# Performance work log

Measured on AMD Instinct MI355X. Metric: run time of the kernel, lower is better.

The kernel has to match this reference:

```python
import jax, jax.numpy as jnp
import numpy as np

DIM = 768
HEADS = 12
HEAD_DIM = DIM // HEADS
SCALE = HEAD_DIM ** (-0.5)


def setup_inputs() -> dict:
    key = jax.random.key(0)
    k1, k2, k3 = jax.random.split(key, 3)
    x = jax.random.normal(k1, (4, 2048, DIM), dtype=jnp.float32)
    # nn.Linear(dim, 3*dim, bias=False): weight [3*dim, dim]
    w_qkv = jax.random.normal(k2, (3 * DIM, DIM), dtype=jnp.float32) * (DIM ** -0.5)
    # nn.Linear(dim, dim) with bias
    w_proj = jax.random.normal(k3, (DIM, DIM), dtype=jnp.float32) * (DIM ** -0.5)
    b_proj = jnp.zeros((DIM,), dtype=jnp.float32)
    return {"x": x, "w_qkv": w_qkv, "w_proj": w_proj, "b_proj": b_proj}


def reference(x, w_qkv, w_proj, b_proj):
    B, N, C = x.shape
    H, D = HEADS, HEAD_DIM
    qkv = jnp.einsum('bnc,oc->bno', x, w_qkv)  # [B,N,3C]
    qkv = qkv.reshape(B, N, 3, H, D).transpose(2, 0, 3, 1, 4)  # [3,B,H,N,D]
    q, k, v = qkv[0], qkv[1], qkv[2]
    attn = jnp.einsum('bhnd,bhmd->bhnm', q, k) * SCALE  # [B,H,N,N]
    attn = jax.nn.softmax(attn, axis=-1)
    attn = jax.nn.softmax(attn, axis=-1)  # double softmax, as in original
    out = jnp.einsum('bhnm,bhmd->bhnd', attn, v)  # [B,H,N,D]
    out = out.transpose(0, 2, 1, 3).reshape(B, N, C)
    return jnp.einsum('bnc,oc->bno', out, w_proj) + b_proj
```

## Files before the change

kernel.cpp:

```cpp
#include <hip/hip_runtime.h>
#include <hip/hip_bf16.h>

#define DIM 768
#define HEADS 12
#define HD 64
#define SEQ 2048
#define BATCH 4
#define BHN 48
#define TOK 8192

#if __has_builtin(__builtin_amdgcn_exp2f)
#define EXP2F __builtin_amdgcn_exp2f
#else
#define EXP2F exp2f
#endif
#define EXP_C 0.1803368801111244f

using short8  = __attribute__((ext_vector_type(8))) short;
using short4v = __attribute__((ext_vector_type(4))) short;
using float4v = __attribute__((ext_vector_type(4))) float;

__device__ __forceinline__ short f2b(float f) {
    union { float f; unsigned u; } v; v.f = f;
    unsigned r = v.u + 0x7FFF + ((v.u >> 16) & 1);
    return (short)(r >> 16);
}
__device__ __forceinline__ float b2f(short s) {
    union { unsigned u; float f; } v;
    v.u = ((unsigned)(unsigned short)s) << 16;
    return v.f;
}
__device__ __forceinline__ unsigned pk2(float a, float b) {
    unsigned r;
    asm("v_cvt_pk_bf16_f32 %0, %1, %2" : "=v"(r) : "v"(a), "v"(b));
    return r;
}

typedef const __attribute__((address_space(1))) unsigned GU;
typedef __attribute__((address_space(3))) unsigned LU;
__device__ __forceinline__ void gload_lds16(const short* g, short* l) {
    __builtin_amdgcn_global_load_lds((GU*)g, (LU*)l, 16, 0, 0);
}

__global__ void cast_all(const float* __restrict__ x, const float* __restrict__ wq,
                         const float* __restrict__ wp,
                         short* __restrict__ xb, short* __restrict__ wqb,
                         short* __restrict__ wpb, float* __restrict__ Vsum,
                         int nx4, int nq4) {
    int i = blockIdx.x * 256 + threadIdx.x;
    if (i < BHN * 64) Vsum[i] = 0.f;
    const float* in; short* out; int j = i;
    if (i < nx4)            { in = x;  out = xb;  }
    else if (i < nx4 + nq4) { in = wq; out = wqb; j = i - nx4; }
    else                    { in = wp; out = wpb; j = i - nx4 - nq4; }
    float4 f = ((const float4*)in)[j];
    short4 o;
    o.x = f2b(f.x); o.y = f2b(f.y); o.z = f2b(f.z); o.w = f2b(f.w);
    ((short4*)out)[j] = o;
}

__global__ __launch_bounds__(256, 3)
void gemm_qkv(const short* __restrict__ A, const short* __restrict__ Bw,
              short* __restrict__ Qw, short* __restrict__ Kw, short* __restrict__ Vw,
              float* __restrict__ Vsum)
{
    __shared__ __align__(16) short As[3][128 * 32];
    __shared__ __align__(16) short Bs[3][128 * 32];

    const int tid  = threadIdx.x;
    const int lane = tid & 63;
    const int wave = tid >> 6;
    const int wm = (wave >> 1) * 64, wn = (wave & 1) * 64;
    const int l15 = lane & 15, quad = lane >> 4;

    const int gid = blockIdx.x;
    const int w   = gid >> 3;
    const int ybl = (gid & 7) * 8 + (w & 7);
    const int xbl = w >> 3;

    const bool vpart = (xbl >= 12);
    const short* rowsP = vpart ? (Bw + 1536 * 768) : A;
    const short* colsP = vpart ? A : Bw;
    const int m0 = vpart ? (xbl - 12) * 128 : ybl * 128;
    const int n0 = vpart ? ybl * 128 : xbl * 128;
    const int K = DIM;

    float4v acc[4][4];
    #pragma unroll
    for (int i = 0; i < 4; i++)
        #pragma unroll
        for (int j = 0; j < 4; j++)
            acc[i][j] = (float4v){0.f, 0.f, 0.f, 0.f};

    const int G0 = wave * 128 + lane;
    const int G1 = G0 + 64;
    const int rA0 = G0 >> 2, cA0 = (G0 & 3) * 8;
    const int rA1 = G1 >> 2, cA1 = (G1 & 3) * 8;
    const int ldsoff = wave * 1024;

    auto STAGE = [&](int t, int buf) {
        const int kc = t * 32;
        gload_lds16(&rowsP[(size_t)(m0 + rA0) * K + kc + cA0], &As[buf][ldsoff]);
        gload_lds16(&rowsP[(size_t)(m0 + rA1) * K + kc + cA1], &As[buf][ldsoff + 512]);
        gload_lds16(&colsP[(size_t)(n0 + rA0) * K + kc + cA0], &Bs[buf][ldsoff]);
        gload_lds16(&colsP[(size_t)(n0 + rA1) * K + kc + cA1], &Bs[buf][ldsoff + 512]);
    };

    STAGE(0, 0);
    STAGE(1, 1);

    int cur = 0, nx2 = 2;
    for (int t = 0; t < 24; t++) {
        if (t < 23) { asm volatile("s_waitcnt vmcnt(4)" ::: "memory"); }
        else        { asm volatile("s_waitcnt vmcnt(0)" ::: "memory"); }
        __builtin_amdgcn_sched_barrier(0);
        __builtin_amdgcn_s_barrier();
        __builtin_amdgcn_sched_barrier(0);

        short8 af[4], bfr[4];
        #pragma unroll
        for (int tt = 0; tt < 4; tt++) {
            af[tt]  = *(const short8*)&As[cur][(wm + tt * 16 + l15) * 32 + quad * 8];
            bfr[tt] = *(const short8*)&Bs[cur][(wn + tt * 16 + l15) * 32 + quad * 8];
        }
        #pragma unroll
        for (int tm = 0; tm < 4; tm++)
            #pragma unroll
            for (int tn = 0; tn < 4; tn++)
                acc[tm][tn] = __builtin_amdgcn_mfma_f32_16x16x32_bf16(af[tm], bfr[tn], acc[tm][tn], 0, 0, 0);

        if (t < 22) STAGE(t + 2, nx2);
        cur = (cur == 2) ? 0 : cur + 1;
        nx2 = (nx2 == 2) ? 0 : nx2 + 1;
    }

    #pragma unroll
    for (int tm = 0; tm < 4; tm++)
        #pragma unroll
        for (int tn = 0; tn < 4; tn++)
            #pragma unroll
            for (int r = 0; r < 4; r++) {
                int row = m0 + wm + tm * 16 + quad * 4 + r;
                int col = n0 + wn + tn * 16 + l15;
                float v = acc[tm][tn][r];
                if (vpart) {
                    int hh = row >> 6, d = row & 63;
                    int b = col >> 11, n = col & 2047;
                    int bh = b * HEADS + hh;
                    int t2 = n >> 6, c2h = (n >> 5) & 1, wk = n & 31;
                    int slot = ((wk & 15) >> 2) * 8 + ((wk & 16) >> 2) + (wk & 3);
                    int g2 = c2h * 4 + (slot >> 3);
                    int gp2 = g2 ^ (d & 7);
                    Vw[(size_t)bh * (SEQ * 64) + t2 * 4096 + d * 64 + gp2 * 8 + (slot & 7)] = f2b(v);
                } else {
                    int hh = (col & 767) >> 6, d = col & 63;
                    int b = row >> 11, n = row & 2047;
                    int bh = b * HEADS + hh;
                    size_t idx = (size_t)bh * (SEQ * 64) + (size_t)n * 64
                               + (((d >> 3) ^ (n & 7)) << 3) + (d & 7);
                    if (col < 768) Qw[idx] = f2b(v * EXP_C);
                    else           Kw[idx] = f2b(v);
                }
            }

    if (vpart) {
        const int bb = n0 >> 11;
        #pragma unroll
        for (int tm = 0; tm < 4; tm++)
            #pragma unroll
            for (int r = 0; r < 4; r++) {
                float s4 = (acc[tm][0][r] + acc[tm][1][r]) + (acc[tm][2][r] + acc[tm][3][r]);
                #pragma unroll
                for (int m = 1; m < 16; m <<= 1) s4 += __shfl_xor(s4, m, 64);
                if (l15 == 0) {
                    int row = m0 + wm + tm * 16 + quad * 4 + r;
                    int hh = row >> 6, d = row & 63;
                    atomicAdd(&Vsum[(bb * HEADS + hh) * 64 + d], s4);
                }
            }
    }
}

__global__ __launch_bounds__(256, 4)
void gemm_proj(const short* __restrict__ A, const short* __restrict__ Bw,
               const float* __restrict__ bias, float* __restrict__ Out)
{
    __shared__ __align__(16) short As[3][128 * 32];
    __shared__ __align__(16) short Bs[3][64 * 32];

    const int tid  = threadIdx.x;
    const int lane = tid & 63;
    const int wave = tid >> 6;
    const int wm = (wave >> 1) * 64, wn = (wave & 1) * 32;
    const int l15 = lane & 15, quad = lane >> 4;

    const int gid = blockIdx.x;
    const int w   = gid >> 3;
    const int ybl = (gid & 7) * 8 + (w & 7);
    const int xbl = w >> 3;
    const int m0 = ybl * 128, n0 = xbl * 64;
    const int K = DIM;

    float4v acc[4][2];
    #pragma unroll
    for (int i = 0; i < 4; i++)
        #pragma unroll
        for (int j = 0; j < 2; j++)
            acc[i][j] = (float4v){0.f, 0.f, 0.f, 0.f};

    const int GA0 = wave * 128 + lane, GA1 = GA0 + 64;
    const int rA0 = GA0 >> 2, cA0 = (GA0 & 3) * 8;
    const int rA1 = GA1 >> 2, cA1 = (GA1 & 3) * 8;
    const int GB0 = wave * 64 + lane;
    const int rB0 = GB0 >> 2, cB0 = (GB0 & 3) * 8;
    const int ldsoffA = wave * 1024, ldsoffB = wave * 512;

    auto STAGE = [&](int t, int buf) {
        const int kc = t * 32;
        gload_lds16(&A [(size_t)(m0 + rA0) * K + kc + cA0], &As[buf][ldsoffA]);
        gload_lds16(&A [(size_t)(m0 + rA1) * K + kc + cA1], &As[buf][ldsoffA + 512]);
        gload_lds16(&Bw[(size_t)(n0 + rB0) * K + kc + cB0], &Bs[buf][ldsoffB]);
    };

    STAGE(0, 0);
    STAGE(1, 1);

    int cur = 0, nx2 = 2;
    for (int t = 0; t < 24; t++) {
        if (t < 23) { asm volatile("s_waitcnt vmcnt(3)" ::: "memory"); }
        else        { asm volatile("s_waitcnt vmcnt(0)" ::: "memory"); }
        __builtin_amdgcn_sched_barrier(0);
        __builtin_amdgcn_s_barrier();
        __builtin_amdgcn_sched_barrier(0);

        short8 af[4], bfr[2];
        #pragma unroll
        for (int tt = 0; tt < 4; tt++)
            af[tt] = *(const short8*)&As[cur][(wm + tt * 16 + l15) * 32 + quad * 8];
        #pragma unroll
        for (int tt = 0; tt < 2; tt++)
            bfr[tt] = *(const short8*)&Bs[cur][(wn + tt * 16 + l15) * 32 + quad * 8];
        #pragma unroll
        for (int tm = 0; tm < 4; tm++)
            #pragma unroll
            for (int tn = 0; tn < 2; tn++)
                acc[tm][tn] = __builtin_amdgcn_mfma_f32_16x16x32_bf16(af[tm], bfr[tn], acc[tm][tn], 0, 0, 0);

        if (t < 22) STAGE(t + 2, nx2);
        cur = (cur == 2) ? 0 : cur + 1;
        nx2 = (nx2 == 2) ? 0 : nx2 + 1;
    }

    #pragma unroll
    for (int tm = 0; tm < 4; tm++)
        #pragma unroll
        for (int tn = 0; tn < 2; tn++)
            #pragma unroll
            for (int r = 0; r < 4; r++) {
                int row = m0 + wm + tm * 16 + quad * 4 + r;
                int col = n0 + wn + tn * 16 + l15;
                Out[(size_t)row * 768 + col] = acc[tm][tn][r] + bias[col];
            }
}

__global__ __launch_bounds__(256, 3)
void attn_kernel(const short* __restrict__ Qw, const short* __restrict__ Kw,
                 const short* __restrict__ Vw, const float* __restrict__ Vsum,
                 short* __restrict__ Ow)
{
    __shared__ __align__(16) short LDS[24576];

    const int tid  = threadIdx.x;
    const int lane = tid & 63, wave = tid >> 6;
    const int l15 = lane & 15, quad = lane >> 4;
    const int r7  = l15 & 7;
    const int bid = blockIdx.x;
    const int ii  = bid >> 3;
    const int bh  = (bid & 7) * 6 + (ii >> 4);
    const int qt  = ii & 15;
    const int wq  = wave * 32;

    const short* Qp = Qw + (size_t)bh * (SEQ * 64) + qt * 8192;
    const short* Kp = Kw + (size_t)bh * (SEQ * 64);
    const short* Vp = Vw + (size_t)bh * (SEQ * 64);

    short8 onesf;
    #pragma unroll
    for (int j = 0; j < 8; j++) onesf[j] = (l15 == 0) ? (short)0x3F80 : (short)0;

    #pragma unroll
    for (int h = 0; h < 4; h++) {
        const int g = wave * 4 + h;
        gload_lds16(&Qp[g * 512 + lane * 8], &LDS[g * 512]);
    }
    __syncthreads();
    short8 aq[2][2];
    #pragma unroll
    for (int nb = 0; nb < 2; nb++)
        #pragma unroll
        for (int kk = 0; kk < 2; kk++) {
            int r = wq + nb * 16 + l15;
            aq[nb][kk] = *(const short8*)&LDS[r * 64 + (((kk * 4 + quad) ^ r7) << 3)];
        }
    __syncthreads();

    float4v Aacc[2][4], Lacc[2];
    #pragma unroll
    for (int mb = 0; mb < 2; mb++) {
        Lacc[mb] = (float4v){0.f, 0.f, 0.f, 0.f};
        #pragma unroll
        for (int t = 0; t < 4; t++) Aacc[mb][t] = (float4v){0.f, 0.f, 0.f, 0.f};
    }

    auto STAGE = [&](int t2, int kbuf) {
        const int kb = kbuf * 4096;
        #pragma unroll
        for (int h = 0; h < 2; h++) {
            const int g = wave * 2 + h;
            gload_lds16(&Kp[(size_t)t2 * 4096 + g * 512 + lane * 8], &LDS[kb + g * 512]);
            gload_lds16(&Vp[(size_t)t2 * 4096 + g * 512 + lane * 8], &LDS[12288 + kb + g * 512]);
        }
    };

    STAGE(0, 0);
    STAGE(1, 1);

    int cur = 0, nx2 = 2;
    for (int kt = 0; kt < 32; kt++) {
        if (kt < 31) { asm volatile("s_waitcnt vmcnt(4)" ::: "memory"); }
        else         { asm volatile("s_waitcnt vmcnt(0)" ::: "memory"); }
        __builtin_amdgcn_sched_barrier(0);
        __builtin_amdgcn_s_barrier();
        __builtin_amdgcn_sched_barrier(0);

        const short* KB = &LDS[cur * 4096];
        const short* VB = &LDS[12288 + cur * 4096];

        #pragma unroll
        for (int c2 = 0; c2 < 2; c2++) {
            union AE { unsigned u[4]; short8 s; };
            AE ae[2];
            #pragma unroll
            for (int tn2 = 0; tn2 < 2; tn2++) {
                const int row = (c2 * 2 + tn2) * 16 + l15;
                const short* rp = &KB[row * 64];
                short8 b0 = *(const short8*)&rp[(quad ^ r7) << 3];
                short8 b1 = *(const short8*)&rp[((4 + quad) ^ r7) << 3];
                #pragma unroll
                for (int nb = 0; nb < 2; nb++) {
                    float4v s = (float4v){0.f, 0.f, 0.f, 0.f};
                    s = __builtin_amdgcn_mfma_f32_16x16x32_bf16(b0, aq[nb][0], s, 0, 0, 0);
                    s = __builtin_amdgcn_mfma_f32_16x16x32_bf16(b1, aq[nb][1], s, 0, 0, 0);
                    ae[nb].u[tn2 * 2]     = pk2(EXP2F(s[0]), EXP2F(s[1]));
                    ae[nb].u[tn2 * 2 + 1] = pk2(EXP2F(s[2]), EXP2F(s[3]));
                }
            }
            __builtin_amdgcn_s_setprio(1);
            Lacc[0] = __builtin_amdgcn_mfma_f32_16x16x32_bf16(ae[0].s, onesf, Lacc[0], 0, 0, 0);
            Lacc[1] = __builtin_amdgcn_mfma_f32_16x16x32_bf16(ae[1].s, onesf, Lacc[1], 0, 0, 0);
            #pragma unroll
            for (int tn = 0; tn < 4; tn++) {
                const int d = tn * 16 + l15;
                short8 bv = *(const short8*)&VB[d * 64 + (((c2 * 4 + quad) ^ r7) << 3)];
                Aacc[0][tn] = __builtin_amdgcn_mfma_f32_16x16x32_bf16(ae[0].s, bv, Aacc[0][tn], 0, 0, 0);
                Aacc[1][tn] = __builtin_amdgcn_mfma_f32_16x16x32_bf16(ae[1].s, bv, Aacc[1][tn], 0, 0, 0);
            }
            __builtin_amdgcn_s_setprio(0);
        }

        if (kt < 30) STAGE(kt + 2, nx2);
        cur = (cur == 2) ? 0 : cur + 1;
        nx2 = (nx2 == 2) ? 0 : nx2 + 1;
    }

    const int b = bh / HEADS, hh = bh - (bh / HEADS) * HEADS;
    #pragma unroll
    for (int mb = 0; mb < 2; mb++)
        #pragma unroll
        for (int r = 0; r < 4; r++) {
            float il = 1.f / __shfl(Lacc[mb][r], lane & 48, 64);
            int row = qt * 128 + wq + mb * 16 + quad * 4 + r;
            int tok = b * SEQ + row;
            #pragma unroll
            for (int tn = 0; tn < 4; tn++) {
                int d = tn * 16 + l15;
                float vs = Vsum[bh * 64 + d];
                float val = (vs + Aacc[mb][tn][r] * il) * (1.f / 2049.f);
                Ow[(size_t)tok * 768 + hh * 64 + d] = f2b(val);
            }
        }
}

extern "C" void kernel_launch(void* const* d_in, const int* in_sizes, int n_in,
                              void* d_out, int out_size, void* d_ws, size_t ws_size,
                              hipStream_t stream) {
    const float* x      = (const float*)d_in[0];
    const float* w_qkv  = (const float*)d_in[1];
    const float* w_proj = (const float*)d_in[2];
    const float* b_proj = (const float*)d_in[3];
    float* out = (float*)d_out;

    char* ws = (char*)d_ws;
    size_t off = 0;
    auto alloc = [&](size_t bytes) {
        void* p = ws + off;
        off += (bytes + 255) & ~(size_t)255;
        return p;
    };
    short* x_bf  = (short*)alloc((size_t)TOK * DIM * 2);
    short* wq_bf = (short*)alloc((size_t)3 * DIM * DIM * 2);
    short* wp_bf = (short*)alloc((size_t)DIM * DIM * 2);
    short* Qw    = (short*)alloc((size_t)BHN * SEQ * 64 * 2);
    short* Kw    = (short*)alloc((size_t)BHN * SEQ * 64 * 2);
    short* Vw    = (short*)alloc((size_t)BHN * SEQ * 64 * 2);
    short* Ow    = (short*)alloc((size_t)TOK * DIM * 2);
    float* Vsum  = (float*)alloc((size_t)BHN * 64 * 4);

    int nx4 = TOK * DIM / 4, nq4 = 3 * DIM * DIM / 4, np4 = DIM * DIM / 4;
    int tot4 = nx4 + nq4 + np4;
    cast_all<<<tot4 / 256, 256, 0, stream>>>(x, w_qkv, w_proj, x_bf, wq_bf, wp_bf, Vsum, nx4, nq4);

    gemm_qkv<<<1152, 256, 0, stream>>>(x_bf, wq_bf, Qw, Kw, Vw, Vsum);

    attn_kernel<<<BHN * 16, 256, 0, stream>>>(Qw, Kw, Vw, Vsum, Ow);

    gemm_proj<<<768, 256, 0, stream>>>(Ow, wp_bf, b_proj, out);
}
```

Measured before the change: 198.7 us.

## Split attention key tile across wave pairs with 64 query rows per wave

Each wave now owns 64 query rows instead of 32 and handles only half of each 64-key tile (one c2 chunk), with wave pairs covering the two halves. Each K and V fragment read from LDS is reused across four query blocks instead of two, which cuts LDS traffic per MFMA. Partial output and row-sum accumulators are combined through LDS at the end, where one wave of each pair writes and the other sums and stores. The cost is doubled accumulator registers per wave, with a risk of spills or lower occupancy under launch_bounds(256,3), plus an extra LDS reduction and barriers in the epilogue.

```diff
diff --git a/kernel.cpp b/kernel.cpp
--- a/kernel.cpp
+++ b/kernel.cpp
@@ -278,7 +278,9 @@
     const int ii  = bid >> 3;
     const int bh  = (bid & 7) * 6 + (ii >> 4);
     const int qt  = ii & 15;
-    const int wq  = wave * 32;
+    const int qh  = wave >> 1;
+    const int kh  = wave & 1;
+    const int wq  = qh * 64;
 
     const short* Qp = Qw + (size_t)bh * (SEQ * 64) + qt * 8192;
     const short* Kp = Kw + (size_t)bh * (SEQ * 64);
@@ -294,9 +296,9 @@
         gload_lds16(&Qp[g * 512 + lane * 8], &LDS[g * 512]);
     }
     __syncthreads();
-    short8 aq[2][2];
-    #pragma unroll
-    for (int nb = 0; nb < 2; nb++)
+    short8 aq[4][2];
+    #pragma unroll
+    for (int nb = 0; nb < 4; nb++)
         #pragma unroll
         for (int kk = 0; kk < 2; kk++) {
             int r = wq + nb * 16 + l15;
@@ -304,12 +306,12 @@
         }
     __syncthreads();
 
-    float4v Aacc[2][4], Lacc[2];
-    #pragma unroll
-    for (int mb = 0; mb < 2; mb++) {
-        Lacc[mb] = (float4v){0.f, 0.f, 0.f, 0.f};
-        #pragma unroll
-        for (int t = 0; t < 4; t++) Aacc[mb][t] = (float4v){0.f, 0.f, 0.f, 0.f};
+    float4v Aacc[4][4], Lacc[4];
+    #pragma unroll
+    for (int nb = 0; nb < 4; nb++) {
+        Lacc[nb] = (float4v){0.f, 0.f, 0.f, 0.f};
+        #pragma unroll
+        for (int t = 0; t < 4; t++) Aacc[nb][t] = (float4v){0.f, 0.f, 0.f, 0.f};
     }
 
     auto STAGE = [&](int t2, int kbuf) {
@@ -335,60 +337,86 @@
 
         const short* KB = &LDS[cur * 4096];
         const short* VB = &LDS[12288 + cur * 4096];
-
-        #pragma unroll
-        for (int c2 = 0; c2 < 2; c2++) {
-            union AE { unsigned u[4]; short8 s; };
-            AE ae[2];
-            #pragma unroll
-            for (int tn2 = 0; tn2 < 2; tn2++) {
-                const int row = (c2 * 2 + tn2) * 16 + l15;
-                const short* rp = &KB[row * 64];
-                short8 b0 = *(const short8*)&rp[(quad ^ r7) << 3];
-                short8 b1 = *(const short8*)&rp[((4 + quad) ^ r7) << 3];
-                #pragma unroll
-                for (int nb = 0; nb < 2; nb++) {
-                    float4v s = (float4v){0.f, 0.f, 0.f, 0.f};
-                    s = __builtin_amdgcn_mfma_f32_16x16x32_bf16(b0, aq[nb][0], s, 0, 0, 0);
-                    s = __builtin_amdgcn_mfma_f32_16x16x32_bf16(b1, aq[nb][1], s, 0, 0, 0);
-                    ae[nb].u[tn2 * 2]     = pk2(EXP2F(s[0]), EXP2F(s[1]));
-                    ae[nb].u[tn2 * 2 + 1] = pk2(EXP2F(s[2]), EXP2F(s[3]));
-                }
-            }
-            __builtin_amdgcn_s_setprio(1);
-            Lacc[0] = __builtin_amdgcn_mfma_f32_16x16x32_bf16(ae[0].s, onesf, Lacc[0], 0, 0, 0);
-            Lacc[1] = __builtin_amdgcn_mfma_f32_16x16x32_bf16(ae[1].s, onesf, Lacc[1], 0, 0, 0);
-            #pragma unroll
-            for (int tn = 0; tn < 4; tn++) {
-                const int d = tn * 16 + l15;
-                short8 bv = *(const short8*)&VB[d * 64 + (((c2 * 4 + quad) ^ r7) << 3)];
-                Aacc[0][tn] = __builtin_amdgcn_mfma_f32_16x16x32_bf16(ae[0].s, bv, Aacc[0][tn], 0, 0, 0);
-                Aacc[1][tn] = __builtin_amdgcn_mfma_f32_16x16x32_bf16(ae[1].s, bv, Aacc[1][tn], 0, 0, 0);
-            }
-            __builtin_amdgcn_s_setprio(0);
-        }
+        const int c2 = kh;
+
+        union AE { unsigned u[4]; short8 s; };
+        AE ae[4];
+        #pragma unroll
+        for (int tn2 = 0; tn2 < 2; tn2++) {
+            const int row = (c2 * 2 + tn2) * 16 + l15;
+            const short* rp = &KB[row * 64];
+            short8 b0 = *(const short8*)&rp[(quad ^ r7) << 3];
+            short8 b1 = *(const short8*)&rp[((4 + quad) ^ r7) << 3];
+            #pragma unroll
+            for (int nb = 0; nb < 4; nb++) {
+                float4v s = (float4v){0.f, 0.f, 0.f, 0.f};
+                s = __builtin_amdgcn_mfma_f32_16x16x32_bf16(b0, aq[nb][0], s, 0, 0, 0);
+                s = __builtin_amdgcn_mfma_f32_16x16x32_bf16(b1, aq[nb][1], s, 0, 0, 0);
+                ae[nb].u[tn2 * 2]     = pk2(EXP2F(s[0]), EXP2F(s[1]));
+                ae[nb].u[tn2 * 2 + 1] = pk2(EXP2F(s[2]), EXP2F(s[3]));
+            }
+        }
+        __builtin_amdgcn_s_setprio(1);
+        #pragma unroll
+        for (int nb = 0; nb < 4; nb++)
+            Lacc[nb] = __builtin_amdgcn_mfma_f32_16x16x32_bf16(ae[nb].s, onesf, Lacc[nb], 0, 0, 0);
+        #pragma unroll
+        for (int tn = 0; tn < 4; tn++) {
+            const int d = tn * 16 + l15;
+            short8 bv = *(const short8*)&VB[d * 64 + (((c2 * 4 + quad) ^ r7) << 3)];
+            #pragma unroll
+            for (int nb = 0; nb < 4; nb++)
+                Aacc[nb][tn] = __builtin_amdgcn_mfma_f32_16x16x32_bf16(ae[nb].s, bv, Aacc[nb][tn], 0, 0, 0);
+        }
+        __builtin_amdgcn_s_setprio(0);
 
         if (kt < 30) STAGE(kt + 2, nx2);
         cur = (cur == 2) ? 0 : cur + 1;
         nx2 = (nx2 == 2) ? 0 : nx2 + 1;
     }
 
-    const int b = bh / HEADS, hh = bh - (bh / HEADS) * HEADS;
-    #pragma unroll
-    for (int mb = 0; mb < 2; mb++)
-        #pragma unroll
-        for (int r = 0; r < 4; r++) {
-            float il = 1.f / __shfl(Lacc[mb][r], lane & 48, 64);
-            int row = qt * 128 + wq + mb * 16 + quad * 4 + r;
-            int tok = b * SEQ + row;
-            #pragma unroll
-            for (int tn = 0; tn < 4; tn++) {
-                int d = tn * 16 + l15;
-                float vs = Vsum[bh * 64 + d];
-                float val = (vs + Aacc[mb][tn][r] * il) * (1.f / 2049.f);
-                Ow[(size_t)tok * 768 + hh * 64 + d] = f2b(val);
-            }
-        }
+    __syncthreads();
+    float* ldsf = (float*)LDS;
+    const int ebase = qh * 5120;
+    if (kh == 1) {
+        #pragma unroll
+        for (int nb = 0; nb < 4; nb++) {
+            #pragma unroll
+            for (int tn = 0; tn < 4; tn++)
+                #pragma unroll
+                for (int r = 0; r < 4; r++)
+                    ldsf[ebase + (nb * 16 + tn * 4 + r) * 64 + lane] = Aacc[nb][tn][r];
+            #pragma unroll
+            for (int r = 0; r < 4; r++)
+                ldsf[ebase + 4096 + (nb * 4 + r) * 64 + lane] = Lacc[nb][r];
+        }
+    }
+    __syncthreads();
+    if (kh == 0) {
+        const int b = bh / HEADS, hh = bh - (bh / HEADS) * HEADS;
+        #pragma unroll
+        for (int nb = 0; nb < 4; nb++) {
+            float il[4];
+            #pragma unroll
+            for (int r = 0; r < 4; r++) {
+                float ls = Lacc[nb][r] + ldsf[ebase + 4096 + (nb * 4 + r) * 64 + lane];
+                il[r] = 1.f / __shfl(ls, lane & 48, 64);
+            }
+            #pragma unroll
+            for (int r = 0; r < 4; r++) {
+                int row = qt * 128 + wq + nb * 16 + quad * 4 + r;
+                int tok = b * SEQ + row;
+                #pragma unroll
+                for (int tn = 0; tn < 4; tn++) {
+                    int d = tn * 16 + l15;
+                    float a = Aacc[nb][tn][r] + ldsf[ebase + (nb * 16 + tn * 4 + r) * 64 + lane];
+                    float vs = Vsum[bh * 64 + d];
+                    float val = (vs + a * il[r]) * (1.f / 2049.f);
+                    Ow[(size_t)tok * 768 + hh * 64 + d] = f2b(val);
+                }
+            }
+        }
+    }
 }
 
 extern "C" void kernel_launch(void* const* d_in, const int* in_sizes, int n_in,
```

Measured after the change: 200.2 us. No clear change (+0.7%).
